# Kernel optimization log

Measured on AMD Instinct MI355X. Metric: run time of the kernel, lower is better.

## Reference

```python
import jax, jax.numpy as jnp
import numpy as np

T = 8192
N = 2048
SPECTRAL_RADIUS = 0.9
WASHOUT = 200


def setup_inputs() -> dict:
    key = jax.random.key(0)
    ku, kin, kres = jax.random.split(key, 3)
    u = jax.random.normal(ku, (T,), dtype=jnp.float32)
    W_in = jax.random.normal(kin, (N,), dtype=jnp.float32)
    W_res = np.asarray(jax.random.normal(kres, (N, N), dtype=jnp.float32))
    # __init__: rescale reservoir to target spectral radius
    spec_rad = float(np.max(np.abs(np.linalg.eigvals(W_res.astype(np.float64)))))
    if spec_rad != 0:
        W_res = W_res * (SPECTRAL_RADIUS / spec_rad)
    return {
        "u": u,
        "W_in": W_in,
        "W_res": jnp.asarray(W_res, dtype=jnp.float32),
        "washout": WASHOUT,
    }


def reference(u, W_in, W_res, washout):
    # Sequential ESN recurrence: x_t = tanh(W_in * u_t + W_res @ x_{t-1})
    n = W_res.shape[0]

    def step(x, u_t):
        x_new = jnp.tanh(W_in * u_t + W_res @ x)  # [N]
        return x_new, x_new

    x0 = jnp.zeros((n,), dtype=W_res.dtype)
    _, X = jax.lax.scan(step, x0, u)  # X: [T, N]
    return X[washout:]  # states after washout (fed to the readout)
```

## Files before the change

### kernel.cpp

```cpp
#include <hip/hip_runtime.h>

#define TSTEPS 8192
#define NDIM   2048
#define NBLK   128
#define NTHR   512
#define RPB    16

typedef float    f32x4 __attribute__((ext_vector_type(4)));
typedef unsigned u32x4 __attribute__((ext_vector_type(4)));

__device__ __forceinline__ unsigned ld_u32_agent(const unsigned* p) {
  return __hip_atomic_load((unsigned*)p, __ATOMIC_RELAXED, __HIP_MEMORY_SCOPE_AGENT);
}
__device__ __forceinline__ void st_u32_agent(unsigned* p, unsigned v) {
  __hip_atomic_store(p, v, __ATOMIC_RELAXED, __HIP_MEMORY_SCOPE_AGENT);
}
__device__ __forceinline__ u32x4 ld_x4_agent(const u32x4* p) {
  u32x4 r;
  asm volatile("global_load_dwordx4 %0, %1, off sc1\n\ts_waitcnt vmcnt(0)"
               : "=v"(r) : "v"(p) : "memory");
  return r;
}
__device__ __forceinline__ void st_x4_agent(u32x4* p, u32x4 v) {
  asm volatile("global_store_dwordx4 %0, %1, off sc1" :: "v"(p), "v"(v) : "memory");
}
__device__ __forceinline__ f32x4 ld_w_sync(const f32x4* p) {
  f32x4 r;
  asm volatile("global_load_dwordx4 %0, %1, off\n\ts_waitcnt vmcnt(0)"
               : "=v"(r) : "v"(p));
  return r;
}

__global__ void __launch_bounds__(NTHR)
__attribute__((amdgpu_waves_per_eu(1, 2))) esn_persistent(
    const float* __restrict__ u,
    const float* __restrict__ W_in,
    const float* __restrict__ W_res,
    const int* __restrict__ washout_p,
    float* __restrict__ out,
    unsigned* __restrict__ ws)
{
  const int tid  = threadIdx.x;
  const int bid  = blockIdx.x;
  const int wave = tid >> 6;
  const int lane = tid & 63;
  const int row0 = bid * RPB + wave * 2;
  const int washout = washout_p[0];

  unsigned* abortw = ws + 144;
  unsigned* buf0   = ws + 256;
  unsigned* buf1   = buf0 + NDIM;

  __shared__ __align__(16) float    x_lds[NDIM];
  __shared__ __align__(16) unsigned xpack_lds[RPB];
  __shared__ __align__(16) float    xval_lds[RPB];
  __shared__ int s_abort;
  if (tid == 0) s_abort = 0;

  const f32x4* Wr0 = (const f32x4*)(W_res + (size_t)row0 * NDIM) + lane;
  const f32x4* Wr1 = (const f32x4*)(W_res + (size_t)(row0 + 1) * NDIM) + lane;
  const f32x4 w00 = ld_w_sync(Wr0 + 0 * 64), w01 = ld_w_sync(Wr0 + 1 * 64);
  const f32x4 w02 = ld_w_sync(Wr0 + 2 * 64), w03 = ld_w_sync(Wr0 + 3 * 64);
  const f32x4 w04 = ld_w_sync(Wr0 + 4 * 64), w05 = ld_w_sync(Wr0 + 5 * 64);
  const f32x4 w06 = ld_w_sync(Wr0 + 6 * 64), w07 = ld_w_sync(Wr0 + 7 * 64);
  const f32x4 w10 = ld_w_sync(Wr1 + 0 * 64), w11 = ld_w_sync(Wr1 + 1 * 64);
  const f32x4 w12 = ld_w_sync(Wr1 + 2 * 64), w13 = ld_w_sync(Wr1 + 3 * 64);
  const f32x4 w14 = ld_w_sync(Wr1 + 4 * 64), w15 = ld_w_sync(Wr1 + 5 * 64);
  const f32x4 w16 = ld_w_sync(Wr1 + 6 * 64), w17 = ld_w_sync(Wr1 + 7 * 64);
  const float win0 = W_in[row0];
  const float win1 = W_in[row0 + 1];

  for (int t = 0; t < TSTEPS; ++t) {
    const u32x4* src = (const u32x4*)((t & 1) ? buf1 : buf0) + tid;
    const unsigned want = (unsigned)t;
    u32x4 r;
    bool ok;
    {
      unsigned g = 0;
      do {
        r = ld_x4_agent(src);
        ok = ((((r.x ^ want) | (r.y ^ want)) |
               ((r.z ^ want) | (r.w ^ want))) & 0xFFFFu) == 0u;
        if (!ok && ((++g & 255u) == 0u)) {
          if (ld_u32_agent(abortw) != 0u) break;
          if (g > (1u << 20)) { st_u32_agent(abortw, 1u); break; }
        }
      } while (!ok);
    }
    if (!ok) s_abort = 1;
    {
      f32x4 xv;
      xv.x = __uint_as_float(r.x & 0xFFFF0000u);
      xv.y = __uint_as_float(r.y & 0xFFFF0000u);
      xv.z = __uint_as_float(r.z & 0xFFFF0000u);
      xv.w = __uint_as_float(r.w & 0xFFFF0000u);
      ((f32x4*)x_lds)[tid] = xv;
    }
    const float ut = u[t];
    __syncthreads();
    if (s_abort) return;

    float a0 = 0.f, b0 = 0.f, a1 = 0.f, b1 = 0.f;
    const f32x4* x4v = (const f32x4*)x_lds + lane;
#define ESN_DOT(WA, WB, K, A, B) { const f32x4 xv = x4v[(K) * 64];            \
      A += WA.x * xv.x; A += WA.y * xv.y; A += WA.z * xv.z; A += WA.w * xv.w; \
      B += WB.x * xv.x; B += WB.y * xv.y; B += WB.z * xv.z; B += WB.w * xv.w; }
    ESN_DOT(w00, w10, 0, a0, a1) ESN_DOT(w01, w11, 1, b0, b1)
    ESN_DOT(w02, w12, 2, a0, a1) ESN_DOT(w03, w13, 3, b0, b1)
    ESN_DOT(w04, w14, 4, a0, a1) ESN_DOT(w05, w15, 5, b0, b1)
    ESN_DOT(w06, w16, 6, a0, a1) ESN_DOT(w07, w17, 7, b0, b1)
#undef ESN_DOT
    const float s0 = a0 + b0;
    const float s1 = a1 + b1;
    const float c0 = s0 + __shfl_xor(s0, 32, 64);
    const float c1 = s1 + __shfl_xor(s1, 32, 64);
    float c = (lane < 32) ? c0 : c1;
#pragma unroll
    for (int off = 16; off > 0; off >>= 1) c += __shfl_xor(c, off, 64);

    if ((lane & 31) == 0) {
      const float wi  = (lane == 0) ? win0 : win1;
      const float pre = wi * ut + c;
      const float e2  = __expf(2.0f * pre);
      const float th  = 1.0f - __fdividef(2.0f, e2 + 1.0f);
      const int   i   = wave * 2 + (lane >> 5);
      xval_lds[i] = th;
      const unsigned b  = __float_as_uint(th);
      const unsigned bf = (b + 0x7fffu + ((b >> 16) & 1u)) & 0xFFFF0000u;
      xpack_lds[i] = bf | (unsigned)(t + 1);
    }
    __syncthreads();

    if (tid < 8) {
      if (tid < 4) {
        u32x4* dst = (u32x4*)(((t + 1) & 1) ? buf1 : buf0) + bid * 4 + tid;
        st_x4_agent(dst, ((const u32x4*)xpack_lds)[tid]);
      } else if (t >= washout) {
        float4* orow = (float4*)(out + (size_t)(t - washout) * NDIM) + bid * 4 + (tid - 4);
        const f32x4 vv = ((const f32x4*)xval_lds)[tid - 4];
        float4 v; v.x = vv.x; v.y = vv.y; v.z = vv.z; v.w = vv.w;
        *orow = v;
      }
    }
  }
}

extern "C" void kernel_launch(void* const* d_in, const int* in_sizes, int n_in,
                              void* d_out, int out_size, void* d_ws, size_t ws_size,
                              hipStream_t stream) {
  const float* u       = (const float*)d_in[0];
  const float* W_in    = (const float*)d_in[1];
  const float* W_res   = (const float*)d_in[2];
  const int*   washout = (const int*)d_in[3];
  float*       out     = (float*)d_out;

  (void)hipMemsetAsync(d_ws, 0, 1024 + 2 * NDIM * 4, stream);

  esn_persistent<<<dim3(NBLK), dim3(NTHR), 0, stream>>>(
      u, W_in, W_res, washout, out, (unsigned*)d_ws);
}
```

Before: 18.23 ms.

## Hand-write pipelined spin-poll in asm and park weights in AGPRs

Replaces the C++ spin-wait on the shared state buffer with an inline-asm loop that keeps two sc1 loads in flight, checks the step tag, masks the values and writes them straight into LDS. The global abort flag is replaced by a single retry counter. The persistent W_res slice moves from VGPRs into accumulation registers via v_accvgpr_write and is read back every step. The aim is lower poll latency on the per-step cross-block handoff and less VGPR pressure, at the cost of extra accvgpr reads each step and hard-coded v40-v49 clobbers that the compiler must honour.

```diff
diff --git a/kernel.cpp b/kernel.cpp
--- a/kernel.cpp
+++ b/kernel.cpp
@@ -9,26 +9,88 @@
 typedef float    f32x4 __attribute__((ext_vector_type(4)));
 typedef unsigned u32x4 __attribute__((ext_vector_type(4)));
 
-__device__ __forceinline__ unsigned ld_u32_agent(const unsigned* p) {
-  return __hip_atomic_load((unsigned*)p, __ATOMIC_RELAXED, __HIP_MEMORY_SCOPE_AGENT);
-}
-__device__ __forceinline__ void st_u32_agent(unsigned* p, unsigned v) {
-  __hip_atomic_store(p, v, __ATOMIC_RELAXED, __HIP_MEMORY_SCOPE_AGENT);
-}
-__device__ __forceinline__ u32x4 ld_x4_agent(const u32x4* p) {
-  u32x4 r;
-  asm volatile("global_load_dwordx4 %0, %1, off sc1\n\ts_waitcnt vmcnt(0)"
-               : "=v"(r) : "v"(p) : "memory");
-  return r;
-}
 __device__ __forceinline__ void st_x4_agent(u32x4* p, u32x4 v) {
   asm volatile("global_store_dwordx4 %0, %1, off sc1" :: "v"(p), "v"(v) : "memory");
 }
-__device__ __forceinline__ f32x4 ld_w_sync(const f32x4* p) {
-  f32x4 r;
-  asm volatile("global_load_dwordx4 %0, %1, off\n\ts_waitcnt vmcnt(0)"
-               : "=v"(r) : "v"(p));
-  return r;
+
+#define W2A(val, A0, A1, A2, A3) do { const f32x4 _w = (val);                \
+  asm volatile("v_accvgpr_write_b32 " A0 ", %0\n\t"                          \
+               "v_accvgpr_write_b32 " A1 ", %1\n\t"                          \
+               "v_accvgpr_write_b32 " A2 ", %2\n\t"                          \
+               "v_accvgpr_write_b32 " A3 ", %3"                              \
+               :: "v"(_w.x), "v"(_w.y), "v"(_w.z), "v"(_w.w)                 \
+               : A0, A1, A2, A3); } while (0)
+
+#define A2V(dst, A0, A1, A2, A3)                                             \
+  asm volatile("v_accvgpr_read_b32 %0, " A0 "\n\t"                           \
+               "v_accvgpr_read_b32 %1, " A1 "\n\t"                           \
+               "v_accvgpr_read_b32 %2, " A2 "\n\t"                           \
+               "v_accvgpr_read_b32 %3, " A3                                  \
+               : "=v"((dst).x), "=v"((dst).y), "=v"((dst).z), "=v"((dst).w))
+
+__device__ __forceinline__ unsigned poll_stage(const u32x4* src, unsigned want,
+                                               unsigned lds_byte) {
+  unsigned cnt;
+  asm volatile(
+    "s_mov_b32 %[ct], 0\n\t"
+    "global_load_dwordx4 v[40:43], %[ad], off sc1\n"
+    "Lpoll%=:\n\t"
+    "global_load_dwordx4 v[44:47], %[ad], off sc1\n\t"
+    "s_waitcnt vmcnt(1)\n\t"
+    "v_xor_b32 v48, %[wt], v40\n\t"
+    "v_xor_b32 v49, %[wt], v41\n\t"
+    "v_or_b32 v48, v48, v49\n\t"
+    "v_xor_b32 v49, %[wt], v42\n\t"
+    "v_or_b32 v48, v48, v49\n\t"
+    "v_xor_b32 v49, %[wt], v43\n\t"
+    "v_or_b32 v48, v48, v49\n\t"
+    "v_and_b32 v48, 0xffff, v48\n\t"
+    "v_cmp_ne_u32 vcc, 0, v48\n\t"
+    "s_cbranch_vccz LdoneA%=\n\t"
+    "s_add_u32 %[ct], %[ct], 1\n\t"
+    "s_cmp_ge_u32 %[ct], 0x100000\n\t"
+    "s_cbranch_scc1 Lfail%=\n\t"
+    "global_load_dwordx4 v[40:43], %[ad], off sc1\n\t"
+    "s_waitcnt vmcnt(1)\n\t"
+    "v_xor_b32 v48, %[wt], v44\n\t"
+    "v_xor_b32 v49, %[wt], v45\n\t"
+    "v_or_b32 v48, v48, v49\n\t"
+    "v_xor_b32 v49, %[wt], v46\n\t"
+    "v_or_b32 v48, v48, v49\n\t"
+    "v_xor_b32 v49, %[wt], v47\n\t"
+    "v_or_b32 v48, v48, v49\n\t"
+    "v_and_b32 v48, 0xffff, v48\n\t"
+    "v_cmp_ne_u32 vcc, 0, v48\n\t"
+    "s_cbranch_vccz LdoneB%=\n\t"
+    "s_add_u32 %[ct], %[ct], 1\n\t"
+    "s_cmp_ge_u32 %[ct], 0x100000\n\t"
+    "s_cbranch_scc1 Lfail%=\n\t"
+    "s_branch Lpoll%=\n"
+    "LdoneA%=:\n\t"
+    "s_waitcnt vmcnt(0)\n\t"
+    "v_and_b32 v44, 0xffff0000, v40\n\t"
+    "v_and_b32 v45, 0xffff0000, v41\n\t"
+    "v_and_b32 v46, 0xffff0000, v42\n\t"
+    "v_and_b32 v47, 0xffff0000, v43\n\t"
+    "ds_write_b128 %[la], v[44:47]\n\t"
+    "s_branch Lend%=\n"
+    "LdoneB%=:\n\t"
+    "s_waitcnt vmcnt(0)\n\t"
+    "v_and_b32 v40, 0xffff0000, v44\n\t"
+    "v_and_b32 v41, 0xffff0000, v45\n\t"
+    "v_and_b32 v42, 0xffff0000, v46\n\t"
+    "v_and_b32 v43, 0xffff0000, v47\n\t"
+    "ds_write_b128 %[la], v[40:43]\n\t"
+    "s_branch Lend%=\n"
+    "Lfail%=:\n\t"
+    "s_waitcnt vmcnt(0)\n"
+    "Lend%=:\n\t"
+    "s_waitcnt lgkmcnt(0)"
+    : [ct]"=&s"(cnt)
+    : [ad]"v"(src), [wt]"v"(want), [la]"v"(lds_byte)
+    : "v40","v41","v42","v43","v44","v45","v46","v47","v48","v49",
+      "vcc","scc","memory");
+  return cnt;
 }
 
 __global__ void __launch_bounds__(NTHR)
@@ -47,9 +109,8 @@
   const int row0 = bid * RPB + wave * 2;
   const int washout = washout_p[0];
 
-  unsigned* abortw = ws + 144;
-  unsigned* buf0   = ws + 256;
-  unsigned* buf1   = buf0 + NDIM;
+  unsigned* buf0 = ws + 256;
+  unsigned* buf1 = buf0 + NDIM;
 
   __shared__ __align__(16) float    x_lds[NDIM];
   __shared__ __align__(16) unsigned xpack_lds[RPB];
@@ -57,59 +118,58 @@
   __shared__ int s_abort;
   if (tid == 0) s_abort = 0;
 
-  const f32x4* Wr0 = (const f32x4*)(W_res + (size_t)row0 * NDIM) + lane;
-  const f32x4* Wr1 = (const f32x4*)(W_res + (size_t)(row0 + 1) * NDIM) + lane;
-  const f32x4 w00 = ld_w_sync(Wr0 + 0 * 64), w01 = ld_w_sync(Wr0 + 1 * 64);
-  const f32x4 w02 = ld_w_sync(Wr0 + 2 * 64), w03 = ld_w_sync(Wr0 + 3 * 64);
-  const f32x4 w04 = ld_w_sync(Wr0 + 4 * 64), w05 = ld_w_sync(Wr0 + 5 * 64);
-  const f32x4 w06 = ld_w_sync(Wr0 + 6 * 64), w07 = ld_w_sync(Wr0 + 7 * 64);
-  const f32x4 w10 = ld_w_sync(Wr1 + 0 * 64), w11 = ld_w_sync(Wr1 + 1 * 64);
-  const f32x4 w12 = ld_w_sync(Wr1 + 2 * 64), w13 = ld_w_sync(Wr1 + 3 * 64);
-  const f32x4 w14 = ld_w_sync(Wr1 + 4 * 64), w15 = ld_w_sync(Wr1 + 5 * 64);
-  const f32x4 w16 = ld_w_sync(Wr1 + 6 * 64), w17 = ld_w_sync(Wr1 + 7 * 64);
+  {
+    const f32x4* Wr0 = (const f32x4*)(W_res + (size_t)row0 * NDIM) + lane;
+    const f32x4* Wr1 = (const f32x4*)(W_res + (size_t)(row0 + 1) * NDIM) + lane;
+    W2A(Wr0[0 * 64], "a0",  "a1",  "a2",  "a3");
+    W2A(Wr0[1 * 64], "a4",  "a5",  "a6",  "a7");
+    W2A(Wr0[2 * 64], "a8",  "a9",  "a10", "a11");
+    W2A(Wr0[3 * 64], "a12", "a13", "a14", "a15");
+    W2A(Wr0[4 * 64], "a16", "a17", "a18", "a19");
+    W2A(Wr0[5 * 64], "a20", "a21", "a22", "a23");
+    W2A(Wr0[6 * 64], "a24", "a25", "a26", "a27");
+    W2A(Wr0[7 * 64], "a28", "a29", "a30", "a31");
+    W2A(Wr1[0 * 64], "a32", "a33", "a34", "a35");
+    W2A(Wr1[1 * 64], "a36", "a37", "a38", "a39");
+    W2A(Wr1[2 * 64], "a40", "a41", "a42", "a43");
+    W2A(Wr1[3 * 64], "a44", "a45", "a46", "a47");
+    W2A(Wr1[4 * 64], "a48", "a49", "a50", "a51");
+    W2A(Wr1[5 * 64], "a52", "a53", "a54", "a55");
+    W2A(Wr1[6 * 64], "a56", "a57", "a58", "a59");
+    W2A(Wr1[7 * 64], "a60", "a61", "a62", "a63");
+  }
   const float win0 = W_in[row0];
   const float win1 = W_in[row0 + 1];
+  const unsigned lds_byte = (unsigned)(size_t)((f32x4*)x_lds + tid);
 
   for (int t = 0; t < TSTEPS; ++t) {
     const u32x4* src = (const u32x4*)((t & 1) ? buf1 : buf0) + tid;
-    const unsigned want = (unsigned)t;
-    u32x4 r;
-    bool ok;
-    {
-      unsigned g = 0;
-      do {
-        r = ld_x4_agent(src);
-        ok = ((((r.x ^ want) | (r.y ^ want)) |
-               ((r.z ^ want) | (r.w ^ want))) & 0xFFFFu) == 0u;
-        if (!ok && ((++g & 255u) == 0u)) {
-          if (ld_u32_agent(abortw) != 0u) break;
-          if (g > (1u << 20)) { st_u32_agent(abortw, 1u); break; }
-        }
-      } while (!ok);
-    }
-    if (!ok) s_abort = 1;
-    {
-      f32x4 xv;
-      xv.x = __uint_as_float(r.x & 0xFFFF0000u);
-      xv.y = __uint_as_float(r.y & 0xFFFF0000u);
-      xv.z = __uint_as_float(r.z & 0xFFFF0000u);
-      xv.w = __uint_as_float(r.w & 0xFFFF0000u);
-      ((f32x4*)x_lds)[tid] = xv;
-    }
+    const unsigned cnt = poll_stage(src, (unsigned)t, lds_byte);
+    if (cnt >= (1u << 20)) s_abort = 1;
     const float ut = u[t];
     __syncthreads();
     if (s_abort) return;
 
     float a0 = 0.f, b0 = 0.f, a1 = 0.f, b1 = 0.f;
     const f32x4* x4v = (const f32x4*)x_lds + lane;
-#define ESN_DOT(WA, WB, K, A, B) { const f32x4 xv = x4v[(K) * 64];            \
-      A += WA.x * xv.x; A += WA.y * xv.y; A += WA.z * xv.z; A += WA.w * xv.w; \
-      B += WB.x * xv.x; B += WB.y * xv.y; B += WB.z * xv.z; B += WB.w * xv.w; }
-    ESN_DOT(w00, w10, 0, a0, a1) ESN_DOT(w01, w11, 1, b0, b1)
-    ESN_DOT(w02, w12, 2, a0, a1) ESN_DOT(w03, w13, 3, b0, b1)
-    ESN_DOT(w04, w14, 4, a0, a1) ESN_DOT(w05, w15, 5, b0, b1)
-    ESN_DOT(w06, w16, 6, a0, a1) ESN_DOT(w07, w17, 7, b0, b1)
-#undef ESN_DOT
+#define ESN_K(K, R0A, R0B, R0C, R0D, R1A, R1B, R1C, R1D, ACC0, ACC1) {       \
+    f32x4 wv0, wv1;                                                          \
+    A2V(wv0, R0A, R0B, R0C, R0D);                                            \
+    A2V(wv1, R1A, R1B, R1C, R1D);                                            \
+    const f32x4 xv = x4v[(K) * 64];                                          \
+    ACC0 += wv0.x * xv.x; ACC0 += wv0.y * xv.y;                              \
+    ACC0 += wv0.z * xv.z; ACC0 += wv0.w * xv.w;                              \
+    ACC1 += wv1.x * xv.x; ACC1 += wv1.y * xv.y;                              \
+    ACC1 += wv1.z * xv.z; ACC1 += wv1.w * xv.w; }
+    ESN_K(0, "a0",  "a1",  "a2",  "a3",  "a32", "a33", "a34", "a35", a0, a1)
+    ESN_K(1, "a4",  "a5",  "a6",  "a7",  "a36", "a37", "a38", "a39", b0, b1)
+    ESN_K(2, "a8",  "a9",  "a10", "a11", "a40", "a41", "a42", "a43", a0, a1)
+    ESN_K(3, "a12", "a13", "a14", "a15", "a44", "a45", "a46", "a47", b0, b1)
+    ESN_K(4, "a16", "a17", "a18", "a19", "a48", "a49", "a50", "a51", a0, a1)
+    ESN_K(5, "a20", "a21", "a22", "a23", "a52", "a53", "a54", "a55", b0, b1)
+    ESN_K(6, "a24", "a25", "a26", "a27", "a56", "a57", "a58", "a59", a0, a1)
+    ESN_K(7, "a28", "a29", "a30", "a31", "a60", "a61", "a62", "a63", b0, b1)
+#undef ESN_K
     const float s0 = a0 + b0;
     const float s1 = a1 + b1;
     const float c0 = s0 + __shfl_xor(s0, 32, 64);
```

Result: slower. 20.19 ms (+10.8%).
